# Performance work log

Measured on AMD Instinct MI355X. Metric: run time of the kernel, lower is better.

The kernel has to match this reference:

```python
import jax, jax.numpy as jnp
import numpy as np

NUM_HEADS = 16
NEG_FILL = -10000.0  # matches torch masked_fill value in source


def setup_inputs() -> dict:
    key = jax.random.key(0)
    ks = jax.random.split(key, 8)
    B, S, H = 4, 2048, 1024
    sc = 1.0 / np.sqrt(H)
    x = jax.random.normal(ks[0], (B, S, H), dtype=jnp.float32)
    L = jax.random.randint(ks[1], (B,), 1, S + 1, dtype=jnp.int64 if jax.config.jax_enable_x64 else jnp.int32)
    Wq = jax.random.normal(ks[2], (H, H), dtype=jnp.float32) * sc
    Wk = jax.random.normal(ks[3], (H, H), dtype=jnp.float32) * sc
    Wv = jax.random.normal(ks[4], (H, H), dtype=jnp.float32) * sc
    bv = jax.random.normal(ks[5], (H,), dtype=jnp.float32) * 0.01
    Wo = jax.random.normal(ks[6], (H, H), dtype=jnp.float32) * sc
    bo = jax.random.normal(ks[7], (H,), dtype=jnp.float32) * 0.01
    return {"x": x, "L": L, "Wq": Wq, "Wk": Wk, "Wv": Wv, "bv": bv, "Wo": Wo, "bo": bo}


def reference(x, L, Wq, Wk, Wv, bv, Wo, bo):
    # AttentionAggregator.forward with L given; dropout in eval mode (identity).
    B, S, H = x.shape
    nh = NUM_HEADS
    dk = H // nh
    # torch nn.Linear: y = x @ W.T + b
    q = (x @ Wq.T).reshape(B, S, nh, dk).transpose(0, 2, 1, 3)  # (B,h,S,dk)
    k = (x @ Wk.T).reshape(B, S, nh, dk).transpose(0, 2, 1, 3)
    v = (x @ Wv.T + bv).reshape(B, S, nh, dk).transpose(0, 2, 1, 3)
    scores = jnp.einsum("bhqd,bhkd->bhqk", q, k) / jnp.sqrt(jnp.float32(dk))
    valid = jnp.arange(S)[None, :] < L[:, None]  # (B,S) True where real token
    scores = jnp.where(valid[:, None, None, :], scores, NEG_FILL)
    attn = jax.nn.softmax(scores, axis=-1)
    ctx = jnp.einsum("bhqk,bhkd->bhqd", attn, v)
    ctx = ctx.transpose(0, 2, 1, 3).reshape(B, S, H)
    attn_out = ctx @ Wo.T + bo  # (B,S,H)
    # masked mean pool over valid positions
    m = valid.astype(x.dtype)  # (B,S)
    pooled = jnp.einsum("bsh,bs->bh", attn_out, m) / m.sum(axis=1, keepdims=True)
    return pooled
```

## Files before the change

kernel.cpp:

```cpp
#include <hip/hip_runtime.h>
#include <hip/hip_bf16.h>
#include <math.h>

constexpr int Bc = 4, Sc = 2048, Hc = 1024, NHc = 16, DKc = 64;

constexpr size_t XHOFF = 0;
constexpr size_t QOFF  = 4194304;
constexpr size_t KOFF  = 8388608;
constexpr size_t WQOFF = 12582912;
constexpr size_t WKOFF = 13107200;
constexpr size_t LIOFF = 13631488;
constexpr size_t WOFF  = 13762560;
constexpr size_t YOFF  = 13893632;
constexpr size_t CSOFF = 13959168;
constexpr size_t YPOFF = 13963264;
constexpr size_t RPOFF = 15011840;
constexpr size_t CPOFF = 15536128;

typedef __attribute__((ext_vector_type(8))) short bf16x8;
typedef __attribute__((ext_vector_type(4))) float f32x4;

__device__ inline short f2bf(float v) {
    __hip_bfloat16 h = __float2bfloat16(v);
    return *reinterpret_cast<short*>(&h);
}

__device__ inline void gld_lds16(const void* g, void* l) {
    __builtin_amdgcn_global_load_lds(
        (const __attribute__((address_space(1))) unsigned int*)g,
        (__attribute__((address_space(3))) unsigned int*)l, 16, 0, 0);
}

__global__ __launch_bounds__(256) void cvt_all_kernel(
    const float* __restrict__ x, const float* __restrict__ Wq,
    const float* __restrict__ Wk, float* __restrict__ ws)
{
    const size_t i = ((size_t)blockIdx.x * 256 + threadIdx.x) * 8;
    const float* src; short* dst; float scale; size_t off;
    if (i < 8388608)       { src = x;  dst = (short*)(ws + XHOFF); off = i;            scale = 1.0f;   }
    else if (i < 9437184)  { src = Wq; dst = (short*)(ws + WQOFF); off = i - 8388608;  scale = 0.125f; }
    else                   { src = Wk; dst = (short*)(ws + WKOFF); off = i - 9437184;  scale = 1.0f;   }
    float4 a = *(const float4*)(src + off);
    float4 b = *(const float4*)(src + off + 4);
    bf16x8 o;
    o[0] = f2bf(a.x * scale); o[1] = f2bf(a.y * scale);
    o[2] = f2bf(a.z * scale); o[3] = f2bf(a.w * scale);
    o[4] = f2bf(b.x * scale); o[5] = f2bf(b.y * scale);
    o[6] = f2bf(b.z * scale); o[7] = f2bf(b.w * scale);
    *(bf16x8*)(dst + off) = o;
}

__global__ __launch_bounds__(256) void proj_mfma_kernel(
    const int* __restrict__ L, float* __restrict__ ws)
{
    const int z  = blockIdx.z;
    const int m0 = blockIdx.y * 128;
    const int n0 = blockIdx.x * 128;
    const int b  = m0 >> 11;
    const int s0 = m0 & 2047;
    const int Lb = L[b];
    if (s0 >= Lb) return;

    const short* __restrict__ A = (const short*)(ws + XHOFF);
    const short* __restrict__ W = (const short*)(ws + (z == 0 ? WQOFF : WKOFF));
    short* __restrict__ Out = (short*)(ws + (z == 0 ? QOFF : KOFF));

    __shared__ __align__(16) short As[128 * 32];
    __shared__ __align__(16) short Bs[128 * 32];

    const int tid  = threadIdx.x;
    const int lane = tid & 63;
    const int wave = tid >> 6;
    const int l16  = lane & 15, quad = lane >> 4;
    const int wm = (wave & 1) * 64, wn = (wave >> 1) * 64;

    const int c0 = tid, c1 = tid + 256;
    const int r0 = c0 >> 2, g0 = (c0 & 3) * 8;
    const int r1 = c1 >> 2, g1 = (c1 & 3) * 8;
    short* lA0 = As + wave * 512;
    short* lA1 = As + 2048 + wave * 512;
    short* lB0 = Bs + wave * 512;
    short* lB1 = Bs + 2048 + wave * 512;

    const f32x4 z4 = {0.f, 0.f, 0.f, 0.f};
    f32x4 acc[4][4];
    #pragma unroll
    for (int i = 0; i < 4; ++i)
        #pragma unroll
        for (int j = 0; j < 4; ++j) acc[i][j] = z4;

    for (int k0 = 0; k0 < Hc; k0 += 32) {
        __syncthreads();
        gld_lds16(A + (size_t)(m0 + r0) * Hc + k0 + g0, lA0);
        gld_lds16(A + (size_t)(m0 + r1) * Hc + k0 + g1, lA1);
        gld_lds16(W + (size_t)(n0 + r0) * Hc + k0 + g0, lB0);
        gld_lds16(W + (size_t)(n0 + r1) * Hc + k0 + g1, lB1);
        __syncthreads();

        bf16x8 af[4], bfr[4];
        #pragma unroll
        for (int mt = 0; mt < 4; ++mt)
            af[mt] = *(const bf16x8*)(As + (wm + mt * 16 + l16) * 32 + quad * 8);
        #pragma unroll
        for (int nt = 0; nt < 4; ++nt)
            bfr[nt] = *(const bf16x8*)(Bs + (wn + nt * 16 + l16) * 32 + quad * 8);
        #pragma unroll
        for (int mt = 0; mt < 4; ++mt)
            #pragma unroll
            for (int nt = 0; nt < 4; ++nt)
                acc[mt][nt] = __builtin_amdgcn_mfma_f32_16x16x32_bf16(
                    af[mt], bfr[nt], acc[mt][nt], 0, 0, 0);
    }

    #pragma unroll
    for (int mt = 0; mt < 4; ++mt) {
        #pragma unroll
        for (int nt = 0; nt < 4; ++nt) {
            const int n = n0 + wn + nt * 16 + l16;
            const int h = n >> 6, d = n & 63;
            #pragma unroll
            for (int r = 0; r < 4; ++r) {
                const int s = s0 + wm + mt * 16 + quad * 4 + r;
                Out[(((size_t)b * NHc + h) * Sc + s) * DKc + d] =
                    f2bf(acc[mt][nt][r]);
            }
        }
    }
}

__global__ __launch_bounds__(256) void rowsum_part_kernel(
    const int* __restrict__ L, float* __restrict__ ws)
{
    const int bh = blockIdx.x;
    const int b  = bh >> 4;
    const int Lb = L[b];
    const int kc0 = blockIdx.z * 512;
    if (blockIdx.y * 128 >= Lb || kc0 >= Lb) return;

    const int tid  = threadIdx.x;
    const int wave = tid >> 6;
    const int lane = tid & 63;
    const int q0 = blockIdx.y * 128 + wave * 32;
    const int l16 = lane & 15, quad = lane >> 4;

    const short* __restrict__ qarr = (const short*)(ws + QOFF) + (size_t)bh * Sc * DKc;
    const short* __restrict__ karr = (const short*)(ws + KOFF) + (size_t)bh * Sc * DKc;

    __shared__ __align__(16) short Ks[128 * 64];

    const short* qrow0 = qarr + (size_t)(q0 + l16) * DKc;
    const short* qrow1 = qarr + (size_t)(q0 + 16 + l16) * DKc;
    const bf16x8 b0lo = *(const bf16x8*)(qrow0 + quad * 8);
    const bf16x8 b0hi = *(const bf16x8*)(qrow0 + 32 + quad * 8);
    const bf16x8 b1lo = *(const bf16x8*)(qrow1 + quad * 8);
    const bf16x8 b1hi = *(const bf16x8*)(qrow1 + 32 + quad * 8);

    const int kend = (kc0 + 512 < Lb) ? kc0 + 512 : Lb;
    float lacc0 = 0.f, lacc1 = 0.f;

    for (int kt = kc0; kt < kend; kt += 128) {
        __syncthreads();
        #pragma unroll
        for (int i = 0; i < 4; ++i) {
            const int s = i * 256 + tid;
            const int row = s >> 3, cc = s & 7, c = cc ^ (row & 7);
            gld_lds16(karr + (size_t)(kt + row) * DKc + c * 8,
                      Ks + (i * 256 + wave * 64) * 8);
        }
        __syncthreads();

        #pragma unroll
        for (int t = 0; t < 8; ++t) {
            const int r = t * 16 + l16;
            const bf16x8 alo = *(const bf16x8*)(Ks + (r * 8 + (quad ^ (r & 7))) * 8);
            const bf16x8 ahi = *(const bf16x8*)(Ks + (r * 8 + ((4 + quad) ^ (r & 7))) * 8);
            f32x4 c0 = {0.f, 0.f, 0.f, 0.f}, c1 = {0.f, 0.f, 0.f, 0.f};
            c0 = __builtin_amdgcn_mfma_f32_16x16x32_bf16(alo, b0lo, c0, 0, 0, 0);
            c0 = __builtin_amdgcn_mfma_f32_16x16x32_bf16(ahi, b0hi, c0, 0, 0, 0);
            c1 = __builtin_amdgcn_mfma_f32_16x16x32_bf16(alo, b1lo, c1, 0, 0, 0);
            c1 = __builtin_amdgcn_mfma_f32_16x16x32_bf16(ahi, b1hi, c1, 0, 0, 0);
            #pragma unroll
            for (int rr = 0; rr < 4; ++rr) {
                const bool kv = (kt + t * 16 + quad * 4 + rr) < kend;
                lacc0 += kv ? __expf(c0[rr]) : 0.f;
                lacc1 += kv ? __expf(c1[rr]) : 0.f;
            }
        }
    }
    lacc0 += __shfl_xor(lacc0, 16, 64); lacc0 += __shfl_xor(lacc0, 32, 64);
    lacc1 += __shfl_xor(lacc1, 16, 64); lacc1 += __shfl_xor(lacc1, 32, 64);
    float* __restrict__ rp = ws + RPOFF + ((size_t)blockIdx.z * 64 + bh) * Sc;
    if (quad == 0) rp[q0 + l16]      = lacc0;
    if (quad == 1) rp[q0 + 16 + l16] = lacc1;
}

__global__ __launch_bounds__(256) void rowsum_reduce_kernel(
    const int* __restrict__ L, float* __restrict__ ws)
{
    const int bh = blockIdx.y;
    const int q  = blockIdx.x * 256 + threadIdx.x;
    const int nc = (L[bh >> 4] + 511) >> 9;
    float acc = 0.f;
    for (int c = 0; c < nc; ++c)
        acc += ws[RPOFF + ((size_t)c * 64 + bh) * Sc + q];
    ws[LIOFF + (size_t)bh * Sc + q] = 1.0f / acc;
}

__global__ __launch_bounds__(256) void colsum_part_kernel(
    const int* __restrict__ L, float* __restrict__ ws)
{
    const int bh = blockIdx.x;
    const int b  = bh >> 4;
    const int Lb = L[b];
    const int qc0 = blockIdx.z * 512;
    if (blockIdx.y * 128 >= Lb || qc0 >= Lb) return;

    const int tid  = threadIdx.x;
    const int wave = tid >> 6;
    const int lane = tid & 63;
    const int k0 = blockIdx.y * 128 + wave * 32;
    const int l16 = lane & 15, quad = lane >> 4;

    const short* __restrict__ qarr = (const short*)(ws + QOFF) + (size_t)bh * Sc * DKc;
    const short* __restrict__ karr = (const short*)(ws + KOFF) + (size_t)bh * Sc * DKc;
    const float* __restrict__ liarr = ws + LIOFF + (size_t)bh * Sc;

    __shared__ __align__(16) short Qs[128 * 64];
    __shared__ __align__(16) float Lis[128];

    const short* krow0 = karr + (size_t)(k0 + l16) * DKc;
    const short* krow1 = karr + (size_t)(k0 + 16 + l16) * DKc;
    const bf16x8 a0lo = *(const bf16x8*)(krow0 + quad * 8);
    const bf16x8 a0hi = *(const bf16x8*)(krow0 + 32 + quad * 8);
    const bf16x8 a1lo = *(const bf16x8*)(krow1 + quad * 8);
    const bf16x8 a1hi = *(const bf16x8*)(krow1 + 32 + quad * 8);

    const int qend = (qc0 + 512 < Lb) ? qc0 + 512 : Lb;
    float w0[4] = {0.f, 0.f, 0.f, 0.f};
    float w1[4] = {0.f, 0.f, 0.f, 0.f};

    for (int qt = qc0; qt < qend; qt += 128) {
        __syncthreads();
        #pragma unroll
        for (int i = 0; i < 4; ++i) {
            const int s = i * 256 + tid;
            const int row = s >> 3, cc = s & 7, c = cc ^ (row & 7);
            gld_lds16(qarr + (size_t)(qt + row) * DKc + c * 8,
                      Qs + (i * 256 + wave * 64) * 8);
        }
        if (tid < 32)
            gld_lds16(liarr + qt + tid * 4, Lis);
        __syncthreads();

        #pragma unroll
        for (int t = 0; t < 8; ++t) {
            const int r = t * 16 + l16;
            const bf16x8 blo = *(const bf16x8*)(Qs + (r * 8 + (quad ^ (r & 7))) * 8);
            const bf16x8 bhi = *(const bf16x8*)(Qs + (r * 8 + ((4 + quad) ^ (r & 7))) * 8);
            const float lv = (qt + r < Lb) ? Lis[r] : 0.f;
            f32x4 c0 = {0.f, 0.f, 0.f, 0.f}, c1 = {0.f, 0.f, 0.f, 0.f};
            c0 = __builtin_amdgcn_mfma_f32_16x16x32_bf16(a0lo, blo, c0, 0, 0, 0);
            c0 = __builtin_amdgcn_mfma_f32_16x16x32_bf16(a0hi, bhi, c0, 0, 0, 0);
            c1 = __builtin_amdgcn_mfma_f32_16x16x32_bf16(a1lo, blo, c1, 0, 0, 0);
            c1 = __builtin_amdgcn_mfma_f32_16x16x32_bf16(a1hi, bhi, c1, 0, 0, 0);
            #pragma unroll
            for (int rr = 0; rr < 4; ++rr) {
                w0[rr] += __expf(c0[rr]) * lv;
                w1[rr] += __expf(c1[rr]) * lv;
            }
        }
    }
    #pragma unroll
    for (int off = 1; off <= 8; off <<= 1) {
        #pragma unroll
        for (int rr = 0; rr < 4; ++rr) {
            w0[rr] += __shfl_xor(w0[rr], off, 64);
            w1[rr] += __shfl_xor(w1[rr], off, 64);
        }
    }
    if (l16 == 0) {
        float* __restrict__ cp = ws + CPOFF + ((size_t)blockIdx.z * 64 + bh) * Sc;
        #pragma unroll
        for (int rr = 0; rr < 4; ++rr) {
            cp[k0 + quad * 4 + rr]      = w0[rr];
            cp[k0 + 16 + quad * 4 + rr] = w1[rr];
        }
    }
}

__global__ __launch_bounds__(256) void colsum_reduce_kernel(
    const int* __restrict__ L, float* __restrict__ ws)
{
    const int bh = blockIdx.y;
    const int k  = blockIdx.x * 256 + threadIdx.x;
    const int nc = (L[bh >> 4] + 511) >> 9;
    float acc = 0.f;
    for (int c = 0; c < nc; ++c)
        acc += ws[CPOFF + ((size_t)c * 64 + bh) * Sc + k];
    ws[WOFF + (size_t)bh * Sc + k] = acc;
}

__global__ __launch_bounds__(256) void yw_part_kernel(
    const float* __restrict__ x, const int* __restrict__ L,
    float* __restrict__ ws)
{
    const int b  = blockIdx.y;
    const int j0 = blockIdx.x * 64;
    const int s0 = blockIdx.z * 128;
    const int Lb = L[b];
    if (s0 >= Lb) return;
    const int js = threadIdx.x & 63;
    const int sl = threadIdx.x >> 6;
    const float* __restrict__ warr = ws + WOFF + (size_t)b * NHc * Sc;
    const float* __restrict__ xb = x + (size_t)b * Sc * Hc;

    __shared__ float wt[128][20];
    __shared__ float red[4][16][64];

    #pragma unroll
    for (int i = 0; i < 8; ++i) {
        const int s = (threadIdx.x & 15) + 16 * i;
        const int h = threadIdx.x >> 4;
        float v = 0.f;
        if (s0 + s < Lb) v = warr[(size_t)h * Sc + s0 + s];
        wt[s][h] = v;
    }
    __syncthreads();

    float acc[16];
    #pragma unroll
    for (int h = 0; h < 16; ++h) acc[h] = 0.f;

    #pragma unroll 4
    for (int s = sl; s < 128; s += 4) {
        const float xv = xb[(size_t)(s0 + s) * Hc + j0 + js];
        const f32x4 wa = *(const f32x4*)&wt[s][0];
        const f32x4 wb = *(const f32x4*)&wt[s][4];
        const f32x4 wc = *(const f32x4*)&wt[s][8];
        const f32x4 wd = *(const f32x4*)&wt[s][12];
        #pragma unroll
        for (int h = 0; h < 4; ++h) acc[h]      += wa[h] * xv;
        #pragma unroll
        for (int h = 0; h < 4; ++h) acc[4 + h]  += wb[h] * xv;
        #pragma unroll
        for (int h = 0; h < 4; ++h) acc[8 + h]  += wc[h] * xv;
        #pragma unroll
        for (int h = 0; h < 4; ++h) acc[12 + h] += wd[h] * xv;
    }
    #pragma unroll
    for (int h = 0; h < 16; ++h) red[sl][h][js] = acc[h];
    __syncthreads();
    if (sl == 0) {
        float* __restrict__ yp = ws + YPOFF +
            ((size_t)blockIdx.z * Bc * NHc + (size_t)b * NHc) * Hc;
        #pragma unroll
        for (int h = 0; h < 16; ++h)
            yp[(size_t)h * Hc + j0 + js] =
                red[0][h][js] + red[1][h][js] + red[2][h][js] + red[3][h][js];
    }
}

__global__ __launch_bounds__(256) void yw_reduce_kernel(
    const int* __restrict__ L, float* __restrict__ ws)
{
    const int b = blockIdx.y;
    const int i = blockIdx.x * 256 + threadIdx.x;
    const int nc = (L[b] + 127) >> 7;
    const float* __restrict__ p = ws + YPOFF + (size_t)b * NHc * Hc + i;
    float acc = 0.f;
    for (int c = 0; c < nc; ++c)
        acc += p[(size_t)c * Bc * NHc * Hc];
    ws[YOFF + (size_t)b * NHc * Hc + i] = acc;
}

__global__ __launch_bounds__(256) void csum_kernel(
    const float* __restrict__ Wv, const float* __restrict__ bv,
    const int* __restrict__ L, float* __restrict__ ws)
{
    const int b = blockIdx.y;
    const int h = blockIdx.x;
    const int n0 = h * 64;
    const int lane = threadIdx.x & 63;
    const int wave = threadIdx.x >> 6;
    const float Lb = (float)L[b];

    __shared__ float ys[1024];
    const float* __restrict__ y = ws + YOFF + ((size_t)b * NHc + h) * Hc;
    for (int i = threadIdx.x; i < 1024; i += 256) ys[i] = y[i];
    __syncthreads();

    f32x4 yv[4];
    #pragma unroll
    for (int p = 0; p < 4; ++p) yv[p] = *(const f32x4*)&ys[p * 256 + lane * 4];

    #pragma unroll
    for (int r = 0; r < 16; ++r) {
        const int n = n0 + wave * 16 + r;
        const float* wrow = Wv + (size_t)n * Hc;
        float a = 0.f;
        #pragma unroll
        for (int p = 0; p < 4; ++p) {
            const f32x4 wv = *(const f32x4*)(wrow + p * 256 + lane * 4);
            a += wv[0]*yv[p][0] + wv[1]*yv[p][1] + wv[2]*yv[p][2] + wv[3]*yv[p][3];
        }
        #pragma unroll
        for (int off = 32; off > 0; off >>= 1) a += __shfl_xor(a, off, 64);
        if (lane == 0)
            ws[CSOFF + (size_t)b * Hc + n] = a + bv[n] * Lb;
    }
}

__global__ __launch_bounds__(256) void out_kernel(
    const float* __restrict__ Wo, const float* __restrict__ bo,
    const int* __restrict__ L, const float* __restrict__ ws,
    float* __restrict__ out)
{
    const int b = blockIdx.y;
    const int o0 = blockIdx.x * 64;
    const int lane = threadIdx.x & 63;
    const int wave = threadIdx.x >> 6;
    const float linv = 1.0f / (float)L[b];

    __shared__ float cs[1024];
    const float* __restrict__ c = ws + CSOFF + (size_t)b * Hc;
    for (int i = threadIdx.x; i < 1024; i += 256) cs[i] = c[i];
    __syncthreads();

    f32x4 cv[4];
    #pragma unroll
    for (int p = 0; p < 4; ++p) cv[p] = *(const f32x4*)&cs[p * 256 + lane * 4];

    #pragma unroll
    for (int r = 0; r < 16; ++r) {
        const int o = o0 + wave * 16 + r;
        const float* wrow = Wo + (size_t)o * Hc;
        float a = 0.f;
        #pragma unroll
        for (int p = 0; p < 4; ++p) {
            const f32x4 wv = *(const f32x4*)(wrow + p * 256 + lane * 4);
            a += wv[0]*cv[p][0] + wv[1]*cv[p][1] + wv[2]*cv[p][2] + wv[3]*cv[p][3];
        }
        #pragma unroll
        for (int off = 32; off > 0; off >>= 1) a += __shfl_xor(a, off, 64);
        if (lane == 0)
            out[(size_t)b * Hc + o] = a * linv + bo[o];
    }
}

extern "C" void kernel_launch(void* const* d_in, const int* in_sizes, int n_in,
                              void* d_out, int out_size, void* d_ws, size_t ws_size,
                              hipStream_t stream)
{
    (void)in_sizes; (void)n_in; (void)out_size; (void)ws_size;
    const float* x  = (const float*)d_in[0];
    const int*   L  = (const int*)d_in[1];
    const float* Wq = (const float*)d_in[2];
    const float* Wk = (const float*)d_in[3];
    const float* Wv = (const float*)d_in[4];
    const float* bv = (const float*)d_in[5];
    const float* Wo = (const float*)d_in[6];
    const float* bo = (const float*)d_in[7];
    float* out = (float*)d_out;
    float* ws  = (float*)d_ws;

    cvt_all_kernel<<<5120, 256, 0, stream>>>(x, Wq, Wk, ws);

    dim3 gp(Hc / 128, (Bc * Sc) / 128, 2);
    proj_mfma_kernel<<<gp, 256, 0, stream>>>(L, ws);

    dim3 gr(Bc * NHc, Sc / 128, 4);
    rowsum_part_kernel<<<gr, 256, 0, stream>>>(L, ws);
    dim3 grr(Sc / 256, Bc * NHc);
    rowsum_reduce_kernel<<<grr, 256, 0, stream>>>(L, ws);

    dim3 gcp(Bc * NHc, Sc / 128, 4);
    colsum_part_kernel<<<gcp, 256, 0, stream>>>(L, ws);
    colsum_reduce_kernel<<<grr, 256, 0, stream>>>(L, ws);

    dim3 gy(Hc / 64, Bc, Sc / 128);
    yw_part_kernel<<<gy, 256, 0, stream>>>(x, L, ws);

    dim3 gyr((NHc * Hc) / 256, Bc);
    yw_reduce_kernel<<<gyr, 256, 0, stream>>>(L, ws);

    dim3 gc(NHc, Bc);
    csum_kernel<<<gc, 256, 0, stream>>>(Wv, bv, L, ws);

    dim3 go(Hc / 64, Bc);
    out_kernel<<<go, 256, 0, stream>>>(Wo, bo, L, ws, out);
}
```

Baseline: 241.4 us.

## Use persistent atomic work-queue kernels for rowsum and colsum partial passes

Replaces the fixed 3D grids of the rowsum and colsum partial kernels, where many blocks exit early for masked tiles, with persistent 1024-block kernels. Each block pulls work items from a global atomic counter and decodes them into only the valid (head, tile, chunk) combinations for the given lengths. A tiny zero kernel resets the counters each call. This aims to cut the launch and scheduling overhead of empty blocks and to balance load, at the cost of an atomic fetch and extra syncs per item plus one more launch.

After: 259.3 us. 7.4% more time.

```diff
diff --git a/kernel.cpp b/kernel.cpp
--- a/kernel.cpp
+++ b/kernel.cpp
@@ -16,6 +16,7 @@
 constexpr size_t YPOFF = 13963264;
 constexpr size_t RPOFF = 15011840;
 constexpr size_t CPOFF = 15536128;
+constexpr size_t ZOFF  = 16060416;
 
 typedef __attribute__((ext_vector_type(8))) short bf16x8;
 typedef __attribute__((ext_vector_type(4))) float f32x4;
@@ -29,6 +30,40 @@
     __builtin_amdgcn_global_load_lds(
         (const __attribute__((address_space(1))) unsigned int*)g,
         (__attribute__((address_space(3))) unsigned int*)l, 16, 0, 0);
+}
+
+__device__ inline void decode_item(const int* L, int it,
+                                   int& bh, int& tile, int& chunk, int& Lb)
+{
+    int rem = it;
+    int b = 0, nt = 0, nc = 0;
+    for (; b < 4; ++b) {
+        const int lb = L[b];
+        nt = (lb + 127) >> 7;
+        nc = (lb + 511) >> 9;
+        const int cnt = 16 * nt * nc;
+        if (rem < cnt) break;
+        rem -= cnt;
+    }
+    Lb = L[b];
+    const int h = rem / (nt * nc);
+    const int r2 = rem - h * (nt * nc);
+    tile  = r2 / nc;
+    chunk = r2 - tile * nc;
+    bh = b * 16 + h;
+}
+
+__device__ inline int total_items(const int* L) {
+    int tot = 0;
+    for (int b = 0; b < 4; ++b) {
+        const int lb = L[b];
+        tot += 16 * ((lb + 127) >> 7) * ((lb + 511) >> 9);
+    }
+    return tot;
+}
+
+__global__ void zero_kernel(float* __restrict__ ws) {
+    ((int*)(ws + ZOFF))[threadIdx.x] = 0;
 }
 
 __global__ __launch_bounds__(256) void cvt_all_kernel(
@@ -128,70 +163,80 @@
     }
 }
 
-__global__ __launch_bounds__(256) void rowsum_part_kernel(
-    const int* __restrict__ L, float* __restrict__ ws)
-{
-    const int bh = blockIdx.x;
-    const int b  = bh >> 4;
-    const int Lb = L[b];
-    const int kc0 = blockIdx.z * 512;
-    if (blockIdx.y * 128 >= Lb || kc0 >= Lb) return;
-
+__global__ __launch_bounds__(256) void rowsum_persist_kernel(
+    const int* __restrict__ L, float* __restrict__ ws)
+{
     const int tid  = threadIdx.x;
     const int wave = tid >> 6;
     const int lane = tid & 63;
-    const int q0 = blockIdx.y * 128 + wave * 32;
     const int l16 = lane & 15, quad = lane >> 4;
-
-    const short* __restrict__ qarr = (const short*)(ws + QOFF) + (size_t)bh * Sc * DKc;
-    const short* __restrict__ karr = (const short*)(ws + KOFF) + (size_t)bh * Sc * DKc;
+    int* __restrict__ counter = (int*)(ws + ZOFF);
 
     __shared__ __align__(16) short Ks[128 * 64];
-
-    const short* qrow0 = qarr + (size_t)(q0 + l16) * DKc;
-    const short* qrow1 = qarr + (size_t)(q0 + 16 + l16) * DKc;
-    const bf16x8 b0lo = *(const bf16x8*)(qrow0 + quad * 8);
-    const bf16x8 b0hi = *(const bf16x8*)(qrow0 + 32 + quad * 8);
-    const bf16x8 b1lo = *(const bf16x8*)(qrow1 + quad * 8);
-    const bf16x8 b1hi = *(const bf16x8*)(qrow1 + 32 + quad * 8);
-
-    const int kend = (kc0 + 512 < Lb) ? kc0 + 512 : Lb;
-    float lacc0 = 0.f, lacc1 = 0.f;
-
-    for (int kt = kc0; kt < kend; kt += 128) {
+    __shared__ int s_item;
+
+    const int tot = total_items(L);
+
+    for (;;) {
         __syncthreads();
-        #pragma unroll
-        for (int i = 0; i < 4; ++i) {
-            const int s = i * 256 + tid;
-            const int row = s >> 3, cc = s & 7, c = cc ^ (row & 7);
-            gld_lds16(karr + (size_t)(kt + row) * DKc + c * 8,
-                      Ks + (i * 256 + wave * 64) * 8);
-        }
+        if (tid == 0) s_item = atomicAdd(counter, 1);
         __syncthreads();
-
-        #pragma unroll
-        for (int t = 0; t < 8; ++t) {
-            const int r = t * 16 + l16;
-            const bf16x8 alo = *(const bf16x8*)(Ks + (r * 8 + (quad ^ (r & 7))) * 8);
-            const bf16x8 ahi = *(const bf16x8*)(Ks + (r * 8 + ((4 + quad) ^ (r & 7))) * 8);
-            f32x4 c0 = {0.f, 0.f, 0.f, 0.f}, c1 = {0.f, 0.f, 0.f, 0.f};
-            c0 = __builtin_amdgcn_mfma_f32_16x16x32_bf16(alo, b0lo, c0, 0, 0, 0);
-            c0 = __builtin_amdgcn_mfma_f32_16x16x32_bf16(ahi, b0hi, c0, 0, 0, 0);
-            c1 = __builtin_amdgcn_mfma_f32_16x16x32_bf16(alo, b1lo, c1, 0, 0, 0);
-            c1 = __builtin_amdgcn_mfma_f32_16x16x32_bf16(ahi, b1hi, c1, 0, 0, 0);
-            #pragma unroll
-            for (int rr = 0; rr < 4; ++rr) {
-                const bool kv = (kt + t * 16 + quad * 4 + rr) < kend;
-                lacc0 += kv ? __expf(c0[rr]) : 0.f;
-                lacc1 += kv ? __expf(c1[rr]) : 0.f;
-            }
-        }
-    }
-    lacc0 += __shfl_xor(lacc0, 16, 64); lacc0 += __shfl_xor(lacc0, 32, 64);
-    lacc1 += __shfl_xor(lacc1, 16, 64); lacc1 += __shfl_xor(lacc1, 32, 64);
-    float* __restrict__ rp = ws + RPOFF + ((size_t)blockIdx.z * 64 + bh) * Sc;
-    if (quad == 0) rp[q0 + l16]      = lacc0;
-    if (quad == 1) rp[q0 + 16 + l16] = lacc1;
+        const int it = s_item;
+        if (it >= tot) return;
+
+        int bh, tile, chunk, Lb;
+        decode_item(L, it, bh, tile, chunk, Lb);
+        const int q0  = tile * 128 + wave * 32;
+        const int kc0 = chunk * 512;
+
+        const short* __restrict__ qarr = (const short*)(ws + QOFF) + (size_t)bh * Sc * DKc;
+        const short* __restrict__ karr = (const short*)(ws + KOFF) + (size_t)bh * Sc * DKc;
+
+        const short* qrow0 = qarr + (size_t)(q0 + l16) * DKc;
+        const short* qrow1 = qarr + (size_t)(q0 + 16 + l16) * DKc;
+        const bf16x8 b0lo = *(const bf16x8*)(qrow0 + quad * 8);
+        const bf16x8 b0hi = *(const bf16x8*)(qrow0 + 32 + quad * 8);
+        const bf16x8 b1lo = *(const bf16x8*)(qrow1 + quad * 8);
+        const bf16x8 b1hi = *(const bf16x8*)(qrow1 + 32 + quad * 8);
+
+        const int kend = (kc0 + 512 < Lb) ? kc0 + 512 : Lb;
+        float lacc0 = 0.f, lacc1 = 0.f;
+
+        for (int kt = kc0; kt < kend; kt += 128) {
+            #pragma unroll
+            for (int i = 0; i < 4; ++i) {
+                const int s = i * 256 + tid;
+                const int row = s >> 3, c = (s & 7) ^ (row & 7);
+                gld_lds16(karr + (size_t)(kt + row) * DKc + c * 8,
+                          Ks + (i * 256 + wave * 64) * 8);
+            }
+            __syncthreads();
+
+            #pragma unroll
+            for (int t = 0; t < 8; ++t) {
+                const int r = t * 16 + l16;
+                const bf16x8 alo = *(const bf16x8*)(Ks + (r * 8 + (quad ^ (r & 7))) * 8);
+                const bf16x8 ahi = *(const bf16x8*)(Ks + (r * 8 + ((4 + quad) ^ (r & 7))) * 8);
+                f32x4 c0 = {0.f, 0.f, 0.f, 0.f}, c1 = {0.f, 0.f, 0.f, 0.f};
+                c0 = __builtin_amdgcn_mfma_f32_16x16x32_bf16(alo, b0lo, c0, 0, 0, 0);
+                c0 = __builtin_amdgcn_mfma_f32_16x16x32_bf16(ahi, b0hi, c0, 0, 0, 0);
+                c1 = __builtin_amdgcn_mfma_f32_16x16x32_bf16(alo, b1lo, c1, 0, 0, 0);
+                c1 = __builtin_amdgcn_mfma_f32_16x16x32_bf16(ahi, b1hi, c1, 0, 0, 0);
+                #pragma unroll
+                for (int rr = 0; rr < 4; ++rr) {
+                    const bool kv = (kt + t * 16 + quad * 4 + rr) < kend;
+                    lacc0 += kv ? __expf(c0[rr]) : 0.f;
+                    lacc1 += kv ? __expf(c1[rr]) : 0.f;
+                }
+            }
+            __syncthreads();
+        }
+        lacc0 += __shfl_xor(lacc0, 16, 64); lacc0 += __shfl_xor(lacc0, 32, 64);
+        lacc1 += __shfl_xor(lacc1, 16, 64); lacc1 += __shfl_xor(lacc1, 32, 64);
+        float* __restrict__ rp = ws + RPOFF + ((size_t)chunk * 64 + bh) * Sc;
+        if (quad == 0) rp[q0 + l16]      = lacc0;
+        if (quad == 1) rp[q0 + 16 + l16] = lacc1;
+    }
 }
 
 __global__ __launch_bounds__(256) void rowsum_reduce_kernel(
@@ -206,84 +251,93 @@
     ws[LIOFF + (size_t)bh * Sc + q] = 1.0f / acc;
 }
 
-__global__ __launch_bounds__(256) void colsum_part_kernel(
-    const int* __restrict__ L, float* __restrict__ ws)
-{
-    const int bh = blockIdx.x;
-    const int b  = bh >> 4;
-    const int Lb = L[b];
-    const int qc0 = blockIdx.z * 512;
-    if (blockIdx.y * 128 >= Lb || qc0 >= Lb) return;
-
+__global__ __launch_bounds__(256) void colsum_persist_kernel(
+    const int* __restrict__ L, float* __restrict__ ws)
+{
     const int tid  = threadIdx.x;
     const int wave = tid >> 6;
     const int lane = tid & 63;
-    const int k0 = blockIdx.y * 128 + wave * 32;
     const int l16 = lane & 15, quad = lane >> 4;
-
-    const short* __restrict__ qarr = (const short*)(ws + QOFF) + (size_t)bh * Sc * DKc;
-    const short* __restrict__ karr = (const short*)(ws + KOFF) + (size_t)bh * Sc * DKc;
-    const float* __restrict__ liarr = ws + LIOFF + (size_t)bh * Sc;
+    int* __restrict__ counter = (int*)(ws + ZOFF) + 1;
 
     __shared__ __align__(16) short Qs[128 * 64];
     __shared__ __align__(16) float Lis[128];
-
-    const short* krow0 = karr + (size_t)(k0 + l16) * DKc;
-    const short* krow1 = karr + (size_t)(k0 + 16 + l16) * DKc;
-    const bf16x8 a0lo = *(const bf16x8*)(krow0 + quad * 8);
-    const bf16x8 a0hi = *(const bf16x8*)(krow0 + 32 + quad * 8);
-    const bf16x8 a1lo = *(const bf16x8*)(krow1 + quad * 8);
-    const bf16x8 a1hi = *(const bf16x8*)(krow1 + 32 + quad * 8);
-
-    const int qend = (qc0 + 512 < Lb) ? qc0 + 512 : Lb;
-    float w0[4] = {0.f, 0.f, 0.f, 0.f};
-    float w1[4] = {0.f, 0.f, 0.f, 0.f};
-
-    for (int qt = qc0; qt < qend; qt += 128) {
+    __shared__ int s_item;
+
+    const int tot = total_items(L);
+
+    for (;;) {
         __syncthreads();
-        #pragma unroll
-        for (int i = 0; i < 4; ++i) {
-            const int s = i * 256 + tid;
-            const int row = s >> 3, cc = s & 7, c = cc ^ (row & 7);
-            gld_lds16(qarr + (size_t)(qt + row) * DKc + c * 8,
-                      Qs + (i * 256 + wave * 64) * 8);
-        }
-        if (tid < 32)
-            gld_lds16(liarr + qt + tid * 4, Lis);
+        if (tid == 0) s_item = atomicAdd(counter, 1);
         __syncthreads();
-
-        #pragma unroll
-        for (int t = 0; t < 8; ++t) {
-            const int r = t * 16 + l16;
-            const bf16x8 blo = *(const bf16x8*)(Qs + (r * 8 + (quad ^ (r & 7))) * 8);
-            const bf16x8 bhi = *(const bf16x8*)(Qs + (r * 8 + ((4 + quad) ^ (r & 7))) * 8);
-            const float lv = (qt + r < Lb) ? Lis[r] : 0.f;
-            f32x4 c0 = {0.f, 0.f, 0.f, 0.f}, c1 = {0.f, 0.f, 0.f, 0.f};
-            c0 = __builtin_amdgcn_mfma_f32_16x16x32_bf16(a0lo, blo, c0, 0, 0, 0);
-            c0 = __builtin_amdgcn_mfma_f32_16x16x32_bf16(a0hi, bhi, c0, 0, 0, 0);
-            c1 = __builtin_amdgcn_mfma_f32_16x16x32_bf16(a1lo, blo, c1, 0, 0, 0);
-            c1 = __builtin_amdgcn_mfma_f32_16x16x32_bf16(a1hi, bhi, c1, 0, 0, 0);
+        const int it = s_item;
+        if (it >= tot) return;
+
+        int bh, tile, chunk, Lb;
+        decode_item(L, it, bh, tile, chunk, Lb);
+        const int k0  = tile * 128 + wave * 32;
+        const int qc0 = chunk * 512;
+
+        const short* __restrict__ qarr = (const short*)(ws + QOFF) + (size_t)bh * Sc * DKc;
+        const short* __restrict__ karr = (const short*)(ws + KOFF) + (size_t)bh * Sc * DKc;
+        const float* __restrict__ liarr = ws + LIOFF + (size_t)bh * Sc;
+
+        const short* krow0 = karr + (size_t)(k0 + l16) * DKc;
+        const short* krow1 = karr + (size_t)(k0 + 16 + l16) * DKc;
+        const bf16x8 a0lo = *(const bf16x8*)(krow0 + quad * 8);
+        const bf16x8 a0hi = *(const bf16x8*)(krow0 + 32 + quad * 8);
+        const bf16x8 a1lo = *(const bf16x8*)(krow1 + quad * 8);
+        const bf16x8 a1hi = *(const bf16x8*)(krow1 + 32 + quad * 8);
+
+        const int qend = (qc0 + 512 < Lb) ? qc0 + 512 : Lb;
+        float w0[4] = {0.f, 0.f, 0.f, 0.f};
+        float w1[4] = {0.f, 0.f, 0.f, 0.f};
+
+        for (int qt = qc0; qt < qend; qt += 128) {
+            #pragma unroll
+            for (int i = 0; i < 4; ++i) {
+                const int s = i * 256 + tid;
+                const int row = s >> 3, c = (s & 7) ^ (row & 7);
+                gld_lds16(qarr + (size_t)(qt + row) * DKc + c * 8,
+                          Qs + (i * 256 + wave * 64) * 8);
+            }
+            if (tid < 32) gld_lds16(liarr + qt + tid * 4, Lis);
+            __syncthreads();
+
+            #pragma unroll
+            for (int t = 0; t < 8; ++t) {
+                const int r = t * 16 + l16;
+                const bf16x8 blo = *(const bf16x8*)(Qs + (r * 8 + (quad ^ (r & 7))) * 8);
+                const bf16x8 bhi = *(const bf16x8*)(Qs + (r * 8 + ((4 + quad) ^ (r & 7))) * 8);
+                const float lv = (qt + r < Lb) ? Lis[r] : 0.f;
+                f32x4 c0 = {0.f, 0.f, 0.f, 0.f}, c1 = {0.f, 0.f, 0.f, 0.f};
+                c0 = __builtin_amdgcn_mfma_f32_16x16x32_bf16(a0lo, blo, c0, 0, 0, 0);
+                c0 = __builtin_amdgcn_mfma_f32_16x16x32_bf16(a0hi, bhi, c0, 0, 0, 0);
+                c1 = __builtin_amdgcn_mfma_f32_16x16x32_bf16(a1lo, blo, c1, 0, 0, 0);
+                c1 = __builtin_amdgcn_mfma_f32_16x16x32_bf16(a1hi, bhi, c1, 0, 0, 0);
+                #pragma unroll
+                for (int rr = 0; rr < 4; ++rr) {
+                    w0[rr] += __expf(c0[rr]) * lv;
+                    w1[rr] += __expf(c1[rr]) * lv;
+                }
+            }
+            __syncthreads();
+        }
+        #pragma unroll
+        for (int off = 1; off <= 8; off <<= 1) {
             #pragma unroll
             for (int rr = 0; rr < 4; ++rr) {
-                w0[rr] += __expf(c0[rr]) * lv;
-                w1[rr] += __expf(c1[rr]) * lv;
-            }
-        }
-    }
-    #pragma unroll
-    for (int off = 1; off <= 8; off <<= 1) {
-        #pragma unroll
-        for (int rr = 0; rr < 4; ++rr) {
-            w0[rr] += __shfl_xor(w0[rr], off, 64);
-            w1[rr] += __shfl_xor(w1[rr], off, 64);
-        }
-    }
-    if (l16 == 0) {
-        float* __restrict__ cp = ws + CPOFF + ((size_t)blockIdx.z * 64 + bh) * Sc;
-        #pragma unroll
-        for (int rr = 0; rr < 4; ++rr) {
-            cp[k0 + quad * 4 + rr]      = w0[rr];
-            cp[k0 + 16 + quad * 4 + rr] = w1[rr];
+                w0[rr] += __shfl_xor(w0[rr], off, 64);
+                w1[rr] += __shfl_xor(w1[rr], off, 64);
+            }
+        }
+        if (l16 == 0) {
+            float* __restrict__ cp = ws + CPOFF + ((size_t)chunk * 64 + bh) * Sc;
+            #pragma unroll
+            for (int rr = 0; rr < 4; ++rr) {
+                cp[k0 + quad * 4 + rr]      = w0[rr];
+                cp[k0 + 16 + quad * 4 + rr] = w1[rr];
+            }
         }
     }
 }
@@ -463,18 +517,17 @@
     float* out = (float*)d_out;
     float* ws  = (float*)d_ws;
 
+    zero_kernel<<<1, 2, 0, stream>>>(ws);
     cvt_all_kernel<<<5120, 256, 0, stream>>>(x, Wq, Wk, ws);
 
     dim3 gp(Hc / 128, (Bc * Sc) / 128, 2);
     proj_mfma_kernel<<<gp, 256, 0, stream>>>(L, ws);
 
-    dim3 gr(Bc * NHc, Sc / 128, 4);
-    rowsum_part_kernel<<<gr, 256, 0, stream>>>(L, ws);
+    rowsum_persist_kernel<<<1024, 256, 0, stream>>>(L, ws);
     dim3 grr(Sc / 256, Bc * NHc);
     rowsum_reduce_kernel<<<grr, 256, 0, stream>>>(L, ws);
 
-    dim3 gcp(Bc * NHc, Sc / 128, 4);
-    colsum_part_kernel<<<gcp, 256, 0, stream>>>(L, ws);
+    colsum_persist_kernel<<<1024, 256, 0, stream>>>(L, ws);
     colsum_reduce_kernel<<<grr, 256, 0, stream>>>(L, ws);
 
     dim3 gy(Hc / 64, Bc, Sc / 128);
```
